# Performance work log

Measured on AMD Instinct MI355X. Metric: run time of the kernel, lower is better.

Reference implementation:

```python
import jax, jax.numpy as jnp
import numpy as np

DN = ('NCHW', 'OIHW', 'NCHW')
EPS = 1e-5


def _mask_time(x, lengths):
    # zero out positions t >= length along the last (time) axis
    T = x.shape[-1]
    valid = jnp.arange(T)[None, None, None, :] < lengths[:, None, None, None]
    return jnp.where(valid, x, jnp.zeros((), x.dtype))


def _conv(x, w, b, stride, pad):
    y = jax.lax.conv_general_dilated(x, w, window_strides=stride,
                                     padding=[(pad[0], pad[0]), (pad[1], pad[1])],
                                     dimension_numbers=DN)
    return y + b[None, :, None, None]


def _bn(x, g, be, m, v):
    inv = jax.lax.rsqrt(v + EPS)
    return (x - m[None, :, None, None]) * (g * inv)[None, :, None, None] + be[None, :, None, None]


def setup_inputs() -> dict:
    key = jax.random.key(0)
    ks = jax.random.split(key, 16)
    f32 = jnp.float32
    return {
        'x': jax.random.normal(ks[0], (16, 1, 161, 1024), f32),
        'x_lengths': jax.random.randint(ks[1], (16,), 1, 512),
        'w1': jax.random.normal(ks[2], (32, 1, 41, 11), f32) * 0.05,
        'b1': jax.random.normal(ks[3], (32,), f32) * 0.05,
        'g1': jax.random.uniform(ks[4], (32,), f32) + 0.5,
        'be1': jax.random.normal(ks[5], (32,), f32) * 0.05,
        'm1': jax.random.normal(ks[6], (32,), f32) * 0.05,
        'v1': jax.random.uniform(ks[7], (32,), f32) + 0.5,
        'w2': jax.random.normal(ks[8], (32, 32, 21, 11), f32) * 0.02,
        'b2': jax.random.normal(ks[9], (32,), f32) * 0.05,
        'g2': jax.random.uniform(ks[10], (32,), f32) + 0.5,
        'be2': jax.random.normal(ks[11], (32,), f32) * 0.05,
        'm2': jax.random.normal(ks[12], (32,), f32) * 0.05,
        'v2': jax.random.uniform(ks[13], (32,), f32) + 0.5,
    }


def reference(x, x_lengths, w1, b1, g1, be1, m1, v1, w2, b2, g2, be2, m2, v2):
    # module 1: conv1 -> mask
    h = _mask_time(_conv(x, w1, b1, (2, 2), (20, 5)), x_lengths)   # [16,32,81,512]
    # module 2: bn1 -> mask
    h = _mask_time(_bn(h, g1, be1, m1, v1), x_lengths)
    # module 3: hardtanh(0,20) -> mask
    h = _mask_time(jnp.clip(h, 0.0, 20.0), x_lengths)
    # module 4: conv2 -> mask
    h = _mask_time(_conv(h, w2, b2, (2, 1), (10, 5)), x_lengths)   # [16,32,41,512]
    # module 5: bn2 -> mask
    h = _mask_time(_bn(h, g2, be2, m2, v2), x_lengths)
    # module 6: hardtanh(0,20) -> mask
    h = _mask_time(jnp.clip(h, 0.0, 20.0), x_lengths)
    return h
```

## Files before the change

kernel.cpp:

```cpp
#include <hip/hip_runtime.h>

typedef __attribute__((ext_vector_type(8))) __bf16 bf16x8;
typedef __attribute__((ext_vector_type(16))) float f32x16;

__device__ __forceinline__ unsigned short f2bf(float f) {
    unsigned int u = __float_as_uint(f);
    unsigned int r = (u + 0x7FFFu + ((u >> 16) & 1u)) >> 16;
    return (unsigned short)r;
}

#define GLL16(gp, lp) \
    __builtin_amdgcn_global_load_lds( \
        (const __attribute__((address_space(1))) unsigned int*)(gp), \
        (__attribute__((address_space(3))) unsigned int*)(lp), 16, 0, 0)

__global__ __launch_bounds__(256) void prep_w1t(const float* __restrict__ w1,
                                                unsigned short* __restrict__ w1t)
{
    const int t = blockIdx.x * 256 + threadIdx.x;
    const int k    = t % 48;
    const int rest = t / 48;
    const int oc   = rest & 31;
    const int kw   = rest >> 5;
    unsigned short v = 0;
    if (k < 41) v = f2bf(w1[(oc * 41 + k) * 11 + kw]);
    w1t[t] = v;
}

__global__ __launch_bounds__(256) void prep_w2f(const float* __restrict__ w2,
                                                unsigned short* __restrict__ w2tf)
{
    const int gid = blockIdx.x * 256 + threadIdx.x;
    const int j  = gid & 7;
    const int l  = (gid >> 3) & 63;
    const int s  = (gid >> 9) & 1;
    const int ti = gid >> 10;
    const int khp = ti / 11;
    const int kw  = ti - khp * 11;
    const int kh  = khp - 2;
    const int oc  = l & 31;
    const int ic  = s * 16 + ((l >> 5) << 3) + j;
    unsigned short v = 0;
    if ((unsigned)kh <= 20u)
        v = f2bf(w2[((oc * 32 + ic) * 21 + kh) * 11 + kw]);
    w2tf[gid] = v;
}

__global__ __launch_bounds__(256) void zero_halo(unsigned short* __restrict__ h1s)
{
    const int id  = blockIdx.x * 256 + threadIdx.x;
    const int c16 = id & 15;
    const int q   = (id >> 4) & 3;
    const int nr  = id >> 6;
    const int c   = c16 < 5 ? c16 : 512 + c16;
    uint4 z = {0u, 0u, 0u, 0u};
    *(uint4*)((char*)h1s + ((size_t)(nr * 4 + q) * 528 + c) * 16) = z;
}

__global__ __launch_bounds__(256) void conv1_mfma(
    const float* __restrict__ x, const int* __restrict__ xlen,
    const unsigned short* __restrict__ w1t,
    const float* __restrict__ b1, const float* __restrict__ g1,
    const float* __restrict__ be1, const float* __restrict__ m1,
    const float* __restrict__ v1,
    unsigned short* __restrict__ h1s)
{
    __shared__ uint4 lds4[2128];
    char* lds = (char*)lds4;

    const int t  = threadIdx.x;
    const int bx = blockIdx.x;
    const int yi = blockIdx.y;
    const int n  = blockIdx.z;
    const int oh0 = ((yi >> 2) << 3) + (yi & 3);
    const int len = xlen[n];

    const int l   = t & 63;
    const int w   = t >> 6;
    const int l31 = l & 31;
    const int lhi = l >> 5;

    char* h8 = (char*)h1s;
    const size_t rowpitch = 33792;

    if (bx * 128 >= len) {
        #pragma unroll
        for (int it = 0; it < 4; ++it) {
            const int idx = t + it * 256;
            const int d1 = idx >> 9;
            const int q  = (idx >> 7) & 3;
            const int cl = idx & 127;
            const int oh = oh0 + 4 * d1;
            if (oh <= 80) {
                uint4 z = {0u, 0u, 0u, 0u};
                *(uint4*)(h8 + (size_t)(n * 81 + oh) * rowpitch + q * 8448
                          + (5 + (bx << 7) + cl) * 16) = z;
            }
        }
        return;
    }

    const int cw   = t & 63;
    const int jrow = t >> 6;
    const int gr0  = 2 * oh0 - 20;
    const int gc0  = bx * 256 - 5;
    const float* xn = x + (size_t)n * 161 * 1024;
    #pragma unroll
    for (int cg = 0; cg < 5; ++cg) {
        const int c = cg * 64 + cw;
        if (c < 266) {
            const int gc = gc0 + c;
            const bool cok = (gc >= 0) && (gc < 1024);
            #pragma unroll
            for (int jj = 0; jj < 2; ++jj) {
                const int j = jrow + 4 * jj;
                if (j < 7) {
                    unsigned int u[4];
                    #pragma unroll
                    for (int q = 0; q < 4; ++q) {
                        const int rA = gr0 + 8 * j + 2 * q;
                        float lo = 0.f, hi = 0.f;
                        if (cok && rA >= 0 && rA < 161)         lo = xn[(size_t)rA * 1024 + gc];
                        if (cok && rA + 1 >= 0 && rA + 1 < 161) hi = xn[(size_t)(rA + 1) * 1024 + gc];
                        u[q] = (unsigned int)f2bf(lo) | ((unsigned int)f2bf(hi) << 16);
                    }
                    uint4 val; val.x = u[0]; val.y = u[1]; val.z = u[2]; val.w = u[3];
                    *(uint4*)(lds + c * 128 + ((j ^ ((c >> 1) & 7)) << 4)) = val;
                }
            }
        }
    }
    __syncthreads();

    const int i = (w << 5) + l31;

    f32x16 acc0 = {}, acc1 = {};
    const char* w1tb = (const char*)w1t;
    #pragma unroll
    for (int kw = 0; kw < 11; ++kw) {
        const char* ap = w1tb + kw * 3072 + l31 * 96 + lhi * 16;
        const bf16x8 a0 = *(const bf16x8*)(ap);
        const bf16x8 a1 = *(const bf16x8*)(ap + 32);
        const bf16x8 a2 = *(const bf16x8*)(ap + 64);
        const int c = 2 * i + kw;
        const char* cb = lds + c * 128;
        const int sw = (c >> 1) & 7;
        const bf16x8 b00 = *(const bf16x8*)(cb + (((0 + lhi) ^ sw) << 4));
        const bf16x8 b01 = *(const bf16x8*)(cb + (((2 + lhi) ^ sw) << 4));
        const bf16x8 b02 = *(const bf16x8*)(cb + (((4 + lhi) ^ sw) << 4));
        const bf16x8 b10 = *(const bf16x8*)(cb + (((1 + lhi) ^ sw) << 4));
        const bf16x8 b11 = *(const bf16x8*)(cb + (((3 + lhi) ^ sw) << 4));
        const bf16x8 b12 = *(const bf16x8*)(cb + (((5 + lhi) ^ sw) << 4));
        acc0 = __builtin_amdgcn_mfma_f32_32x32x16_bf16(a0, b00, acc0, 0, 0, 0);
        acc0 = __builtin_amdgcn_mfma_f32_32x32x16_bf16(a1, b01, acc0, 0, 0, 0);
        acc0 = __builtin_amdgcn_mfma_f32_32x32x16_bf16(a2, b02, acc0, 0, 0, 0);
        acc1 = __builtin_amdgcn_mfma_f32_32x32x16_bf16(a0, b10, acc1, 0, 0, 0);
        acc1 = __builtin_amdgcn_mfma_f32_32x32x16_bf16(a1, b11, acc1, 0, 0, 0);
        acc1 = __builtin_amdgcn_mfma_f32_32x32x16_bf16(a2, b12, acc1, 0, 0, 0);
    }

    __syncthreads();
    const int ow  = bx * 128 + i;
    const bool vmask = ow < len;
    #pragma unroll
    for (int d1 = 0; d1 < 2; ++d1) {
        const int oh = oh0 + 4 * d1;
        if (oh <= 80) {
            #pragma unroll
            for (int q = 0; q < 4; ++q) {
                float vv[4];
                #pragma unroll
                for (int rr = 0; rr < 4; ++rr) {
                    const int reg = (q << 2) + rr;
                    const int oc  = rr + (q << 3) + (lhi << 2);
                    const float s = g1[oc] * rsqrtf(v1[oc] + 1e-5f);
                    float val = ((d1 ? acc1[reg] : acc0[reg]) + b1[oc] - m1[oc]) * s + be1[oc];
                    val = fminf(fmaxf(val, 0.f), 20.f);
                    vv[rr] = vmask ? val : 0.f;
                }
                uint2 pk;
                pk.x = (unsigned int)f2bf(vv[0]) | ((unsigned int)f2bf(vv[1]) << 16);
                pk.y = (unsigned int)f2bf(vv[2]) | ((unsigned int)f2bf(vv[3]) << 16);
                *(uint2*)(lds + (((d1 << 2) + q) << 11) + i * 16 + lhi * 8) = pk;
            }
        }
    }
    __syncthreads();
    #pragma unroll
    for (int it = 0; it < 4; ++it) {
        const int idx = t + it * 256;
        const int d1 = idx >> 9;
        const int q  = (idx >> 7) & 3;
        const int cl = idx & 127;
        const int oh = oh0 + 4 * d1;
        if (oh <= 80) {
            const uint4 v = *(const uint4*)(lds + (((d1 << 2) + q) << 11) + cl * 16);
            *(uint4*)(h8 + (size_t)(n * 81 + oh) * rowpitch + q * 8448
                      + (5 + (bx << 7) + cl) * 16) = v;
        }
    }
}

__global__ __launch_bounds__(256, 2) void conv2_v5(
    const unsigned short* __restrict__ h1s, const unsigned short* __restrict__ w2tf,
    const int* __restrict__ xlen,
    const float* __restrict__ b2, const float* __restrict__ g2,
    const float* __restrict__ be2, const float* __restrict__ m2,
    const float* __restrict__ v2, float* __restrict__ out)
{
    __shared__ char lbuf[32768];

    const int t   = threadIdx.x;
    const int w   = t >> 6;
    const int l   = t & 63;
    const int l31 = l & 31;
    const int lhi = l >> 5;
    const int cg  = w >> 1;
    const int s   = w & 1;

    const int bid  = blockIdx.x;
    const int lb   = (bid & 7) * 168 + (bid >> 3);
    const int n    = lb / 84;
    const int r2   = lb - n * 84;
    const int by   = r2 >> 2;
    const int bx   = r2 & 3;

    const int ow0 = bx << 7;
    const int len = xlen[n];

    if (ow0 >= len) {
        const int j   = w >> 1;
        const int cgz = w & 1;
        const int oh2 = 2 * by + j;
        if (oh2 <= 40) {
            #pragma unroll
            for (int g = 0; g < 2; ++g) {
                const int ow = ow0 + (cgz << 6) + (g << 5) + l31;
                #pragma unroll
                for (int reg = 0; reg < 16; ++reg) {
                    const int oc = (reg & 3) + ((reg >> 2) << 3) + (lhi << 2);
                    out[((size_t)(n * 32 + oc) * 41 + oh2) * 512 + ow] = 0.f;
                }
            }
        }
        return;
    }

    const int rlo = (4 * by - 10 > 0) ? 4 * by - 10 : 0;
    const int rhi = (4 * by + 12 < 80) ? 4 * by + 12 : 80;

    f32x16 acc[2][2] = {};

    const char* h8 = (const char*)h1s;
    const size_t rowpitch = 33792;
    const char* nb = h8 + (size_t)(n * 81) * rowpitch + (size_t)(ow0 << 4);

    #define STAGE(r, buf) do { \
        const char* g_ = nb + (size_t)(r) * rowpitch + w * 8448; \
        char* d_ = lbuf + (buf) * 9216 + w * 2304; \
        GLL16(g_ + l * 16,        d_ + l * 16); \
        GLL16(g_ + 1024 + l * 16, d_ + 1024 + l * 16); \
        if (l < 16) GLL16(g_ + 2048 + l * 16, d_ + 2048 + l * 16); \
    } while (0)

    STAGE(rlo, 0);
    __syncthreads();

    const char* w8v = (const char*)w2tf;
    int cur = 0;
    for (int r = rlo; r <= rhi; ++r) {
        if (r < rhi) STAGE(r + 1, cur ^ 1);
        const char* lb8 = lbuf + cur * 9216;
        const int khb = r - 4 * by + 10;
        #pragma unroll
        for (int kw = 0; kw < 11; ++kw) {
            const char* bp = lb8 + (2 * s + lhi) * 2304 + ((cg << 6) + l31 + kw) * 16;
            const bf16x8 B0 = *(const bf16x8*)(bp);
            const bf16x8 B1 = *(const bf16x8*)(bp + 512);
            #pragma unroll
            for (int j = 0; j < 2; ++j) {
                const int khp = khb + 2 - 2 * j;
                const bf16x8 A = *(const bf16x8*)(w8v
                    + (size_t)(((khp * 11 + kw) * 2 + s) << 10) + (l << 4));
                acc[j][0] = __builtin_amdgcn_mfma_f32_32x32x16_bf16(A, B0, acc[j][0], 0, 0, 0);
                acc[j][1] = __builtin_amdgcn_mfma_f32_32x32x16_bf16(A, B1, acc[j][1], 0, 0, 0);
            }
        }
        __syncthreads();
        cur ^= 1;
    }
    #undef STAGE

    if (s == 1) {
        #pragma unroll
        for (int j = 0; j < 2; ++j) {
            #pragma unroll
            for (int f = 0; f < 2; ++f) {
                char* dst = lbuf + ((((cg << 1) + j) << 1) + f) * 4096 + l * 16;
                #pragma unroll
                for (int q = 0; q < 4; ++q) {
                    float4 v;
                    v.x = acc[j][f][q * 4 + 0]; v.y = acc[j][f][q * 4 + 1];
                    v.z = acc[j][f][q * 4 + 2]; v.w = acc[j][f][q * 4 + 3];
                    *(float4*)(dst + q * 1024) = v;
                }
            }
        }
    }
    __syncthreads();
    if (s == 1) return;

    #pragma unroll
    for (int j = 0; j < 2; ++j) {
        const int oh2 = 2 * by + j;
        if (oh2 <= 40) {
            #pragma unroll
            for (int f = 0; f < 2; ++f) {
                const char* src = lbuf + ((((cg << 1) + j) << 1) + f) * 4096 + l * 16;
                float pr[16];
                #pragma unroll
                for (int q = 0; q < 4; ++q) {
                    const float4 v = *(const float4*)(src + q * 1024);
                    pr[q * 4 + 0] = v.x; pr[q * 4 + 1] = v.y;
                    pr[q * 4 + 2] = v.z; pr[q * 4 + 3] = v.w;
                }
                const int ow = ow0 + (cg << 6) + (f << 5) + l31;
                const bool valid = ow < len;
                #pragma unroll
                for (int reg = 0; reg < 16; ++reg) {
                    const int oc = (reg & 3) + ((reg >> 2) << 3) + (lhi << 2);
                    const float sc = g2[oc] * rsqrtf(v2[oc] + 1e-5f);
                    float val = (acc[j][f][reg] + pr[reg] + b2[oc] - m2[oc]) * sc + be2[oc];
                    val = fminf(fmaxf(val, 0.f), 20.f);
                    if (!valid) val = 0.f;
                    out[((size_t)(n * 32 + oc) * 41 + oh2) * 512 + ow] = val;
                }
            }
        }
    }
}

extern "C" void kernel_launch(void* const* d_in, const int* in_sizes, int n_in,
                              void* d_out, int out_size, void* d_ws, size_t ws_size,
                              hipStream_t stream) {
    const float* x    = (const float*)d_in[0];
    const int*   xlen = (const int*)  d_in[1];
    const float* w1   = (const float*)d_in[2];
    const float* b1   = (const float*)d_in[3];
    const float* g1   = (const float*)d_in[4];
    const float* be1  = (const float*)d_in[5];
    const float* m1   = (const float*)d_in[6];
    const float* v1   = (const float*)d_in[7];
    const float* w2   = (const float*)d_in[8];
    const float* b2   = (const float*)d_in[9];
    const float* g2   = (const float*)d_in[10];
    const float* be2  = (const float*)d_in[11];
    const float* m2   = (const float*)d_in[12];
    const float* v2   = (const float*)d_in[13];
    float* out = (float*)d_out;

    unsigned short* h1s  = (unsigned short*)d_ws;
    unsigned short* w2tf = h1s + 21897216;
    unsigned short* w1t  = w2tf + 281600;

    prep_w1t<<<dim3(66),   dim3(256), 0, stream>>>(w1, w1t);
    prep_w2f<<<dim3(1100), dim3(256), 0, stream>>>(w2, w2tf);
    zero_halo<<<dim3(324), dim3(256), 0, stream>>>(h1s);
    conv1_mfma<<<dim3(4, 41, 16), dim3(256), 0, stream>>>(
        x, xlen, w1t, b1, g1, be1, m1, v1, h1s);
    conv2_v5<<<dim3(1344), dim3(256), 0, stream>>>(
        h1s, w2tf, xlen, b2, g2, be2, m2, v2, out);
}
```

Before: 220.4 us.

## Deepen conv2 LDS pipeline to four buffers with one barrier per row

Replaces the double-buffered row staging in conv2 with a 4-slot ring that prefetches two rows ahead. It uses an explicit vmcnt wait plus one barrier per iteration instead of two __syncthreads, aiming to hide global-to-LDS latency and cut sync overhead. It also changes the block-to-tile mapping to a multiplicative permutation (bid*605 mod 1344) for different load spreading across CUs. LDS grows slightly (36 KB), and the hand-tuned vmcnt count must match the number of outstanding loads per stage for correctness.

```diff
diff --git a/kernel.cpp b/kernel.cpp
--- a/kernel.cpp
+++ b/kernel.cpp
@@ -201,14 +201,14 @@
     }
 }
 
-__global__ __launch_bounds__(256, 2) void conv2_v5(
+__global__ __launch_bounds__(256, 2) void conv2_v7(
     const unsigned short* __restrict__ h1s, const unsigned short* __restrict__ w2tf,
     const int* __restrict__ xlen,
     const float* __restrict__ b2, const float* __restrict__ g2,
     const float* __restrict__ be2, const float* __restrict__ m2,
     const float* __restrict__ v2, float* __restrict__ out)
 {
-    __shared__ char lbuf[32768];
+    __shared__ char lbuf[4][9216];
 
     const int t   = threadIdx.x;
     const int w   = t >> 6;
@@ -219,7 +219,7 @@
     const int s   = w & 1;
 
     const int bid  = blockIdx.x;
-    const int lb   = (bid & 7) * 168 + (bid >> 3);
+    const int lb   = (bid * 605) % 1344;
     const int n    = lb / 84;
     const int r2   = lb - n * 84;
     const int by   = r2 >> 2;
@@ -257,20 +257,27 @@
 
     #define STAGE(r, buf) do { \
         const char* g_ = nb + (size_t)(r) * rowpitch + w * 8448; \
-        char* d_ = lbuf + (buf) * 9216 + w * 2304; \
+        char* d_ = &lbuf[buf][0] + w * 2304; \
         GLL16(g_ + l * 16,        d_ + l * 16); \
         GLL16(g_ + 1024 + l * 16, d_ + 1024 + l * 16); \
         if (l < 16) GLL16(g_ + 2048 + l * 16, d_ + 2048 + l * 16); \
     } while (0)
 
-    STAGE(rlo, 0);
-    __syncthreads();
+    STAGE(rlo,     0);
+    STAGE(rlo + 1, 1);
+    STAGE(rlo + 2, 2);
 
     const char* w8v = (const char*)w2tf;
-    int cur = 0;
     for (int r = rlo; r <= rhi; ++r) {
-        if (r < rhi) STAGE(r + 1, cur ^ 1);
-        const char* lb8 = lbuf + cur * 9216;
+        {
+            const int rs = (r + 2 <= rhi) ? r + 2 : rhi;
+            if (r > rlo) STAGE(rs, (r - rlo + 2) & 3);
+        }
+        asm volatile("s_waitcnt vmcnt(6)" ::: "memory");
+        __builtin_amdgcn_s_barrier();
+        __builtin_amdgcn_sched_barrier(0);
+
+        const char* lb8 = &lbuf[(r - rlo) & 3][0];
         const int khb = r - 4 * by + 10;
         #pragma unroll
         for (int kw = 0; kw < 11; ++kw) {
@@ -286,17 +293,17 @@
                 acc[j][1] = __builtin_amdgcn_mfma_f32_32x32x16_bf16(A, B1, acc[j][1], 0, 0, 0);
             }
         }
-        __syncthreads();
-        cur ^= 1;
     }
     #undef STAGE
 
+    __syncthreads();
+    char* red = &lbuf[0][0];
     if (s == 1) {
         #pragma unroll
         for (int j = 0; j < 2; ++j) {
             #pragma unroll
             for (int f = 0; f < 2; ++f) {
-                char* dst = lbuf + ((((cg << 1) + j) << 1) + f) * 4096 + l * 16;
+                char* dst = red + ((((cg << 1) + j) << 1) + f) * 4096 + l * 16;
                 #pragma unroll
                 for (int q = 0; q < 4; ++q) {
                     float4 v;
@@ -316,7 +323,7 @@
         if (oh2 <= 40) {
             #pragma unroll
             for (int f = 0; f < 2; ++f) {
-                const char* src = lbuf + ((((cg << 1) + j) << 1) + f) * 4096 + l * 16;
+                const char* src = red + ((((cg << 1) + j) << 1) + f) * 4096 + l * 16;
                 float pr[16];
                 #pragma unroll
                 for (int q = 0; q < 4; ++q) {
@@ -368,6 +375,6 @@
     zero_halo<<<dim3(324), dim3(256), 0, stream>>>(h1s);
     conv1_mfma<<<dim3(4, 41, 16), dim3(256), 0, stream>>>(
         x, xlen, w1t, b1, g1, be1, m1, v1, h1s);
-    conv2_v5<<<dim3(1344), dim3(256), 0, stream>>>(
+    conv2_v7<<<dim3(1344), dim3(256), 0, stream>>>(
         h1s, w2tf, xlen, b2, g2, be2, m2, v2, out);
 }
```

New measurement: 243.9 us. +10.7%, slower.
